# Kernel tuning notes

Measured on AMD Instinct MI355X. Metric: run time of the kernel, lower is better.

## Reference

```python
import jax, jax.numpy as jnp
import numpy as np

B, S, H, HD = 8, 1024, 16, 64
D = H * HD
NINF = -10000.0
EPS = 1e-6


def setup_inputs() -> dict:
    key = jax.random.key(0)
    ks = jax.random.split(key, 6)
    std = 0.02
    return {
        "x": jax.random.normal(ks[0], (B, S, D), jnp.float32),
        "mask": jax.random.randint(ks[1], (B, S), 0, 2, jnp.int32),
        "wq": jax.random.normal(ks[2], (D, D), jnp.float32) * std,
        "bq": jnp.zeros((D,), jnp.float32),
        "wk": jax.random.normal(ks[3], (D, D), jnp.float32) * std,
        "bk": jnp.zeros((D,), jnp.float32),
        "wv": jax.random.normal(ks[4], (D, D), jnp.float32) * std,
        "bv": jnp.zeros((D,), jnp.float32),
        "wo": jax.random.normal(ks[5], (D, D), jnp.float32) * std,
        "bo": jnp.zeros((D,), jnp.float32),
        "gamma": jnp.ones((D,), jnp.float32),
        "beta": jnp.zeros((D,), jnp.float32),
    }


def _heads(t):
    # [B,S,D] -> [B,H,S,HD]
    return t.reshape(t.shape[0], t.shape[1], H, HD).transpose(0, 2, 1, 3)


def _layernorm(x, gamma, beta):
    mu = jnp.mean(x, -1, keepdims=True)
    var = jnp.mean(jnp.square(x - mu), -1, keepdims=True)
    return (x - mu) * jax.lax.rsqrt(var + EPS) * gamma + beta


def reference(x, mask, wq, bq, wk, bk, wv, bv, wo, bo, gamma, beta):
    q = _heads(x @ wq + bq)
    k = _heads(x @ wk + bk)
    v = _heads(x @ wv + bv)
    scores = jnp.einsum("bhqd,bhkd->bhqk", q, k) / np.sqrt(HD).astype(np.float32)
    # padding mask broadcast over key axis: 1 = masked
    scores = scores + mask.astype(jnp.float32)[:, None, None, :] * NINF
    attn = jax.nn.softmax(scores, axis=-1)
    ctx = jnp.einsum("bhqk,bhkd->bhqd", attn, v)  # [B,H,S,HD]
    ctx = ctx.transpose(0, 2, 1, 3).reshape(B, S, D)
    out = _layernorm(x + ctx @ wo + bo, gamma, beta)
    return out
```

## Files before the change

### kernel.cpp

```cpp
#include <hip/hip_runtime.h>
#include <stdint.h>

typedef unsigned short u16;
typedef unsigned int u32;
typedef __bf16 b16x8 __attribute__((ext_vector_type(8)));
typedef float f32x4 __attribute__((ext_vector_type(4)));

#define B_ 8
#define S_ 1024
#define H_ 16
#define HD_ 64
#define D_ 1024
#define M_ 8192

__device__ __forceinline__ u16 f2bf(float f) {
  u32 u = __float_as_uint(f);
  return (u16)((u + 0x7fffu + ((u >> 16) & 1u)) >> 16);
}
__device__ __forceinline__ u16 bfbits(float f) {
  union {
    __bf16 b;
    u16 u;
  } c;
  c.b = (__bf16)f;
  return c.u;
}

__device__ __forceinline__ f32x4 mfma16(b16x8 a, b16x8 b, f32x4 c) {
  return __builtin_amdgcn_mfma_f32_16x16x32_bf16(a, b, c, 0, 0, 0);
}

__device__ __forceinline__ void cp16(const u16* g, u16* l) {
  __builtin_amdgcn_global_load_lds(
      (const __attribute__((address_space(1))) u32*)(g),
      (__attribute__((address_space(3))) u32*)(l), 16, 0, 0);
}

__global__ __launch_bounds__(1024) void wconv_kernel(
    const float* __restrict__ w0, const float* __restrict__ w1,
    const float* __restrict__ w2, const float* __restrict__ w3,
    u16* __restrict__ t0, u16* __restrict__ t1, u16* __restrict__ t2,
    u16* __restrict__ t3) {
  __shared__ float tile[32][33];
  const int z = blockIdx.z;
  const float* src = (z == 0) ? w0 : (z == 1) ? w1 : (z == 2) ? w2 : w3;
  u16* dst = (z == 0) ? t0 : (z == 1) ? t1 : (z == 2) ? t2 : t3;
  const int tx = threadIdx.x, ty = threadIdx.y;
  const int x0 = blockIdx.x * 32, y0 = blockIdx.y * 32;
  tile[ty][tx] = src[(size_t)(y0 + ty) * D_ + x0 + tx];
  __syncthreads();
  dst[(size_t)(x0 + ty) * D_ + y0 + tx] = f2bf(tile[tx][ty]);
}

__global__ __launch_bounds__(256) void xconv_kernel(const float* __restrict__ x,
                                                    u16* __restrict__ xb) {
  const size_t i = ((size_t)blockIdx.x * 256 + threadIdx.x) * 4;
  const float4 v = *(const float4*)(x + i);
  u16 o[4] = {f2bf(v.x), f2bf(v.y), f2bf(v.z), f2bf(v.w)};
  uint2 pack;
  pack.x = ((u32)o[1] << 16) | o[0];
  pack.y = ((u32)o[3] << 16) | o[2];
  *(uint2*)(xb + i) = pack;
}

#define BM_ 256
#define BN_ 128
#define BK_ 64
#define ABUF_ 16384
#define BBUF_ 8192
#define BUFSZ_ (ABUF_ + BBUF_)

__device__ __forceinline__ void gemm256x128_mainloop(
    const u16* __restrict__ A, const u16* __restrict__ BT, int K, int m0,
    int n0, u16* lds, f32x4 (&acc)[8][2]) {
  const int t = threadIdx.x;
  const int lane = t & 63;
  const int l15 = lane & 15;
  const int q4 = lane >> 4;
  const int w = t >> 6;
  const int wm = w >> 2;
  const int wn = w & 3;

  const f32x4 zero = {0.f, 0.f, 0.f, 0.f};
#pragma unroll
  for (int mt = 0; mt < 8; ++mt)
#pragma unroll
    for (int nt = 0; nt < 2; ++nt) acc[mt][nt] = zero;

  const int rbase = t >> 3;
  const int scol = ((t & 7) ^ (rbase & 7)) * 8;
  const u16* Ag = A + (size_t)(m0 + rbase) * K + scol;
  const u16* Bg = BT + (size_t)(n0 + rbase) * K + scol;
  const int sx = l15 & 7;

  auto STAGE = [&](int kt, int bufi) {
    u16* Ab = lds + bufi * BUFSZ_;
    u16* Bb = Ab + ABUF_;
    const int k0 = kt * BK_;
#pragma unroll
    for (int c = 0; c < 4; ++c)
      cp16(Ag + (size_t)(c * 64) * K + k0, Ab + c * 4096 + t * 8);
#pragma unroll
    for (int c = 0; c < 2; ++c)
      cp16(Bg + (size_t)(c * 64) * K + k0, Bb + c * 4096 + t * 8);
  };

  const int NT = K / BK_;
  STAGE(0, 0);
  STAGE(1, 1);

  int cur = 0;
  for (int kt = 0; kt < NT; ++kt) {
    if (kt + 2 < NT) {
      int nb = cur + 2;
      if (nb >= 3) nb -= 3;
      STAGE(kt + 2, nb);
    }
    if (kt + 2 < NT)
      asm volatile("s_waitcnt vmcnt(12)" ::: "memory");
    else if (kt + 1 < NT)
      asm volatile("s_waitcnt vmcnt(6)" ::: "memory");
    else
      asm volatile("s_waitcnt vmcnt(0)" ::: "memory");
    asm volatile("s_barrier" ::: "memory");

    const u16* Ab = lds + cur * BUFSZ_;
    const u16* Bb = Ab + ABUF_;

#pragma unroll
    for (int kk = 0; kk < 2; ++kk) {
      b16x8 af[8], bf2[2];
      const int cc = ((kk * 4 + q4) ^ sx) * 8;
#pragma unroll
      for (int mt = 0; mt < 8; ++mt)
        af[mt] = *(const b16x8*)(Ab + (wm * 128 + mt * 16 + l15) * 64 + cc);
#pragma unroll
      for (int nt = 0; nt < 2; ++nt)
        bf2[nt] = *(const b16x8*)(Bb + (wn * 32 + nt * 16 + l15) * 64 + cc);
      asm volatile("s_barrier" ::: "memory");
      __builtin_amdgcn_s_setprio(1);
#pragma unroll
      for (int mt = 0; mt < 8; ++mt) {
        acc[mt][0] = mfma16(af[mt], bf2[0], acc[mt][0]);
        acc[mt][1] = mfma16(af[mt], bf2[1], acc[mt][1]);
      }
      __builtin_amdgcn_s_setprio(0);
      asm volatile("s_barrier" ::: "memory");
    }
    ++cur;
    if (cur == 3) cur = 0;
  }
}

__global__ __launch_bounds__(512, 2) void qkv_gemm_kernel(
    const u16* __restrict__ xb, const u16* __restrict__ wt3,
    const float* __restrict__ bq, const float* __restrict__ bk,
    const float* __restrict__ bv, u16* __restrict__ Q, u16* __restrict__ Kb,
    u16* __restrict__ VT) {
  __shared__ __align__(16) u16 lds[3 * BUFSZ_];
  const int wg = blockIdx.x;
  const int xcd = wg & 7;
  const int s = wg >> 3;
  const int by = xcd * 4 + (s & 3);
  const int bx = s >> 2;
  const int m0 = by * 256;
  const int n0 = bx * 128;

  f32x4 acc[8][2];
  gemm256x128_mainloop(xb, wt3, D_, m0, n0, lds, acc);

  const int t = threadIdx.x;
  const int lane = t & 63, w = t >> 6;
  const int l15 = lane & 15, q4 = lane >> 4;
  const int wm = w >> 2, wn = w & 3;

  const int z = n0 >> 10;
  u16* out = (z == 0) ? Q : (z == 1) ? Kb : VT;
  const float* bias = (z == 0) ? bq : (z == 1) ? bk : bv;

  for (int nt = 0; nt < 2; ++nt) {
    const int nf = n0 + wn * 32 + nt * 16 + l15;
    const int n1 = nf & 1023;
    const float bias_v = bias[n1];
    const int h = n1 >> 6, hd = n1 & 63;
    for (int mt = 0; mt < 8; ++mt) {
      for (int r = 0; r < 4; ++r) {
        const int m = m0 + wm * 128 + mt * 16 + q4 * 4 + r;
        const int b = m >> 10, ss = m & 1023;
        const float v = acc[mt][nt][r] + bias_v;
        size_t idx;
        if (z < 2)
          idx = (((size_t)(b * H_ + h)) * S_ + ss) * HD_ + hd;
        else
          idx = (((size_t)(b * H_ + h)) * HD_ + hd) * S_ + ss;
        out[idx] = f2bf(v);
      }
    }
  }
}

#define PAD_ 68
#define QPAD_ 72
__global__ __launch_bounds__(256) void attn_kernel(
    const u16* __restrict__ Q, const u16* __restrict__ Kb,
    const u16* __restrict__ VT, const int* __restrict__ mask,
    u16* __restrict__ ctx) {
  __shared__ __align__(16) u16 QPlds[64 * QPAD_];
  __shared__ __align__(16) u16 Klds[64 * PAD_];
  __shared__ __align__(16) u16 Vlds[64 * PAD_];
  __shared__ __align__(16) float Mlds[1024];

  const int t = threadIdx.x;
  const int lane = t & 63, w = t >> 6;
  const int l15 = lane & 15, q4 = lane >> 4;
  const int id = blockIdx.x;
  const int bh = id & 127;
  const int b = bh >> 4, h = bh & 15;
  const int q0 = (id >> 7) * 64;

  const u16* Qbh = Q + (size_t)bh * S_ * HD_;
  const u16* Kbh = Kb + (size_t)bh * S_ * HD_;
  const u16* Vbh = VT + (size_t)bh * S_ * HD_;
  const int* maskb = mask + b * S_;

  const int srow = t >> 3, scol = (t & 7) * 8;
  {
    b16x8 q0v = *(const b16x8*)(Qbh + (size_t)(q0 + srow) * HD_ + scol);
    b16x8 q1v = *(const b16x8*)(Qbh + (size_t)(q0 + srow + 32) * HD_ + scol);
    const int4 mv = *(const int4*)(maskb + t * 4);
    *(b16x8*)(QPlds + srow * QPAD_ + scol) = q0v;
    *(b16x8*)(QPlds + (srow + 32) * QPAD_ + scol) = q1v;
    float4 mf;
    mf.x = -14427.0f * (float)mv.x;
    mf.y = -14427.0f * (float)mv.y;
    mf.z = -14427.0f * (float)mv.z;
    mf.w = -14427.0f * (float)mv.w;
    *(float4*)(Mlds + t * 4) = mf;
  }
  __syncthreads();
  b16x8 aq[2];
  aq[0] = *(const b16x8*)(QPlds + (w * 16 + l15) * QPAD_ + q4 * 8);
  aq[1] = *(const b16x8*)(QPlds + (w * 16 + l15) * QPAD_ + 32 + q4 * 8);

  const f32x4 zero = {0.f, 0.f, 0.f, 0.f};
  f32x4 acc[4];
  for (int nt = 0; nt < 4; ++nt) acc[nt] = zero;
  float lsum = 0.f;
  u16* Pw = QPlds + w * 16 * QPAD_;
  const float c1 = 0.18033688f;

  b16x8 kv0 = *(const b16x8*)(Kbh + (size_t)srow * HD_ + scol);
  b16x8 kv1 = *(const b16x8*)(Kbh + (size_t)(srow + 32) * HD_ + scol);
  b16x8 vv0 = *(const b16x8*)(Vbh + (size_t)srow * S_ + scol);
  b16x8 vv1 = *(const b16x8*)(Vbh + (size_t)(srow + 32) * S_ + scol);

  for (int j = 0; j < 16; ++j) {
    const int key0 = j * 64;
    __syncthreads();
    *(b16x8*)(Klds + srow * PAD_ + scol) = kv0;
    *(b16x8*)(Klds + (srow + 32) * PAD_ + scol) = kv1;
    *(b16x8*)(Vlds + srow * PAD_ + scol) = vv0;
    *(b16x8*)(Vlds + (srow + 32) * PAD_ + scol) = vv1;
    __syncthreads();

    if (j < 15) {
      const int kn = key0 + 64;
      kv0 = *(const b16x8*)(Kbh + (size_t)(kn + srow) * HD_ + scol);
      kv1 = *(const b16x8*)(Kbh + (size_t)(kn + srow + 32) * HD_ + scol);
      vv0 = *(const b16x8*)(Vbh + (size_t)srow * S_ + kn + scol);
      vv1 = *(const b16x8*)(Vbh + (size_t)(srow + 32) * S_ + kn + scol);
    }

    f32x4 sf[4];
    for (int nt = 0; nt < 4; ++nt) sf[nt] = zero;
    for (int kk = 0; kk < 2; ++kk)
      for (int nt = 0; nt < 4; ++nt) {
        b16x8 bk =
            *(const b16x8*)(Klds + (nt * 16 + l15) * PAD_ + kk * 32 + q4 * 8);
        sf[nt] = mfma16(bk, aq[kk], sf[nt]);
      }

    for (int nt = 0; nt < 4; ++nt) {
      const float4 mk = *(const float4*)(Mlds + key0 + nt * 16 + q4 * 4);
      float p0 = __builtin_amdgcn_exp2f(sf[nt][0] * c1 + mk.x);
      float p1 = __builtin_amdgcn_exp2f(sf[nt][1] * c1 + mk.y);
      float p2 = __builtin_amdgcn_exp2f(sf[nt][2] * c1 + mk.z);
      float p3 = __builtin_amdgcn_exp2f(sf[nt][3] * c1 + mk.w);
      lsum += (p0 + p1) + (p2 + p3);
      uint2 pk;
      pk.x = ((u32)bfbits(p1) << 16) | bfbits(p0);
      pk.y = ((u32)bfbits(p3) << 16) | bfbits(p2);
      *(uint2*)(Pw + l15 * QPAD_ + nt * 16 + q4 * 4) = pk;
    }
    asm volatile("s_waitcnt lgkmcnt(0)" ::: "memory");

    for (int kk = 0; kk < 2; ++kk) {
      b16x8 bp = *(const b16x8*)(Pw + l15 * QPAD_ + kk * 32 + q4 * 8);
      for (int nt = 0; nt < 4; ++nt) {
        b16x8 vb =
            *(const b16x8*)(Vlds + (nt * 16 + l15) * PAD_ + kk * 32 + q4 * 8);
        acc[nt] = mfma16(vb, bp, acc[nt]);
      }
    }
  }

  lsum += __shfl_xor(lsum, 16);
  lsum += __shfl_xor(lsum, 32);
  const float inv = 1.0f / lsum;

  const int srw = q0 + w * 16 + l15;
  u16* crow = ctx + ((size_t)(b * S_ + srw)) * D_ + h * 64;
  for (int nt = 0; nt < 4; ++nt) {
    uint2 pk;
    pk.x = ((u32)bfbits(acc[nt][1] * inv) << 16) | bfbits(acc[nt][0] * inv);
    pk.y = ((u32)bfbits(acc[nt][3] * inv) << 16) | bfbits(acc[nt][2] * inv);
    *(uint2*)(crow + nt * 16 + q4 * 4) = pk;
  }
}

__global__ __launch_bounds__(512, 2) void out_gemm_kernel(
    const u16* __restrict__ ctx, const u16* __restrict__ wto,
    const float* __restrict__ bo, const float* __restrict__ x,
    float* __restrict__ y) {
  __shared__ __align__(16) u16 lds[3 * BUFSZ_];
  const int wg = blockIdx.x;
  const int xcd = wg & 7;
  const int s = wg >> 3;
  const int by = xcd * 4 + (s & 3);
  const int bx = s >> 2;
  const int m0 = by * 256, n0 = bx * 128;

  f32x4 acc[8][2];
  gemm256x128_mainloop(ctx, wto, D_, m0, n0, lds, acc);

  const int t = threadIdx.x;
  const int lane = t & 63, w = t >> 6;
  const int l15 = lane & 15, q4 = lane >> 4;
  const int wm = w >> 2, wn = w & 3;

  for (int nt = 0; nt < 2; ++nt) {
    const int n = n0 + wn * 32 + nt * 16 + l15;
    const float bias = bo[n];
    for (int mt = 0; mt < 8; ++mt) {
      for (int r = 0; r < 4; ++r) {
        const int m = m0 + wm * 128 + mt * 16 + q4 * 4 + r;
        y[(size_t)m * D_ + n] = acc[mt][nt][r] + bias + x[(size_t)m * D_ + n];
      }
    }
  }
}

__global__ __launch_bounds__(256) void ln_kernel(const float* __restrict__ y,
                                                 const float* __restrict__ g,
                                                 const float* __restrict__ be,
                                                 float* __restrict__ out) {
  const int row = blockIdx.x, t = threadIdx.x;
  const float* yr = y + (size_t)row * D_;
  const float4 v = *(const float4*)(yr + t * 4);
  float s = v.x + v.y + v.z + v.w;
  float ss = v.x * v.x + v.y * v.y + v.z * v.z + v.w * v.w;
  for (int off = 1; off < 64; off <<= 1) {
    s += __shfl_xor(s, off);
    ss += __shfl_xor(ss, off);
  }
  __shared__ float red[8];
  const int w = t >> 6, lane = t & 63;
  if (lane == 0) {
    red[w] = s;
    red[4 + w] = ss;
  }
  __syncthreads();
  s = red[0] + red[1] + red[2] + red[3];
  ss = red[4] + red[5] + red[6] + red[7];
  const float mu = s * (1.f / 1024.f);
  const float var = ss * (1.f / 1024.f) - mu * mu;
  const float rs = rsqrtf(var + 1e-6f);
  const int c = t * 4;
  const float4 gv = *(const float4*)(g + c);
  const float4 bv = *(const float4*)(be + c);
  float4 o;
  o.x = (v.x - mu) * rs * gv.x + bv.x;
  o.y = (v.y - mu) * rs * gv.y + bv.y;
  o.z = (v.z - mu) * rs * gv.z + bv.z;
  o.w = (v.w - mu) * rs * gv.w + bv.w;
  *(float4*)(out + (size_t)row * D_ + c) = o;
}

extern "C" void kernel_launch(void* const* d_in, const int* in_sizes, int n_in,
                              void* d_out, int out_size, void* d_ws,
                              size_t ws_size, hipStream_t stream) {
  const float* x = (const float*)d_in[0];
  const int* mask = (const int*)d_in[1];
  const float* wq = (const float*)d_in[2];
  const float* bq = (const float*)d_in[3];
  const float* wk = (const float*)d_in[4];
  const float* bk = (const float*)d_in[5];
  const float* wv = (const float*)d_in[6];
  const float* bv = (const float*)d_in[7];
  const float* wo = (const float*)d_in[8];
  const float* bo = (const float*)d_in[9];
  const float* gamma = (const float*)d_in[10];
  const float* beta = (const float*)d_in[11];
  float* out = (float*)d_out;

  char* ws = (char*)d_ws;
  const size_t MB = 1024ull * 1024ull;
  u16* wtq = (u16*)(ws + 0 * MB);
  u16* wtk = (u16*)(ws + 2 * MB);
  u16* wtv = (u16*)(ws + 4 * MB);
  u16* wto = (u16*)(ws + 6 * MB);
  u16* xb = (u16*)(ws + 8 * MB);
  u16* ctx = (u16*)(ws + 8 * MB);
  u16* Qb = (u16*)(ws + 24 * MB);
  u16* Kb = (u16*)(ws + 40 * MB);
  u16* VTb = (u16*)(ws + 56 * MB);
  float* y = (float*)(ws + 24 * MB);

  wconv_kernel<<<dim3(32, 32, 4), dim3(32, 32), 0, stream>>>(
      wq, wk, wv, wo, wtq, wtk, wtv, wto);
  xconv_kernel<<<8192, 256, 0, stream>>>(x, xb);
  qkv_gemm_kernel<<<768, 512, 0, stream>>>(xb, wtq, bq, bk, bv, Qb, Kb, VTb);
  attn_kernel<<<2048, 256, 0, stream>>>(Qb, Kb, VTb, mask, ctx);
  out_gemm_kernel<<<256, 512, 0, stream>>>(ctx, wto, bo, x, y);
  ln_kernel<<<8192, 256, 0, stream>>>(y, gamma, beta, out);
}
```

Before: 301.6 us.

## Use 256x256 tiles with interleaved quadrant prefetch in QKV GEMM

```diff
diff --git a/kernel.cpp b/kernel.cpp
--- a/kernel.cpp
+++ b/kernel.cpp
@@ -63,29 +63,22 @@
   *(uint2*)(xb + i) = pack;
 }
 
-#define BM_ 256
-#define BN_ 128
-#define BK_ 64
-#define ABUF_ 16384
-#define BBUF_ 8192
-#define BUFSZ_ (ABUF_ + BBUF_)
-
-__device__ __forceinline__ void gemm256x128_mainloop(
-    const u16* __restrict__ A, const u16* __restrict__ BT, int K, int m0,
-    int n0, u16* lds, f32x4 (&acc)[8][2]) {
+__device__ __forceinline__ void gemm256sq_mainloop(
+    const u16* __restrict__ A, const u16* __restrict__ BT, int m0, int n0,
+    u16* lds, f32x4 (&acc)[8][4]) {
   const int t = threadIdx.x;
   const int lane = t & 63;
-  const int l15 = lane & 15;
-  const int q4 = lane >> 4;
+  const int l15 = lane & 15, q4 = lane >> 4;
   const int w = t >> 6;
   const int wm = w >> 2;
   const int wn = w & 3;
+  const int K = D_;
 
   const f32x4 zero = {0.f, 0.f, 0.f, 0.f};
 #pragma unroll
-  for (int mt = 0; mt < 8; ++mt)
-#pragma unroll
-    for (int nt = 0; nt < 2; ++nt) acc[mt][nt] = zero;
+  for (int mf = 0; mf < 8; ++mf)
+#pragma unroll
+    for (int nf = 0; nf < 4; ++nf) acc[mf][nf] = zero;
 
   const int rbase = t >> 3;
   const int scol = ((t & 7) ^ (rbase & 7)) * 8;
@@ -93,62 +86,124 @@
   const u16* Bg = BT + (size_t)(n0 + rbase) * K + scol;
   const int sx = l15 & 7;
 
-  auto STAGE = [&](int kt, int bufi) {
-    u16* Ab = lds + bufi * BUFSZ_;
-    u16* Bb = Ab + ABUF_;
-    const int k0 = kt * BK_;
-#pragma unroll
-    for (int c = 0; c < 4; ++c)
-      cp16(Ag + (size_t)(c * 64) * K + k0, Ab + c * 4096 + t * 8);
-#pragma unroll
-    for (int c = 0; c < 2; ++c)
-      cp16(Bg + (size_t)(c * 64) * K + k0, Bb + c * 4096 + t * 8);
-  };
-
-  const int NT = K / BK_;
-  STAGE(0, 0);
-  STAGE(1, 1);
-
-  int cur = 0;
-  for (int kt = 0; kt < NT; ++kt) {
-    if (kt + 2 < NT) {
-      int nb = cur + 2;
-      if (nb >= 3) nb -= 3;
-      STAGE(kt + 2, nb);
-    }
-    if (kt + 2 < NT)
-      asm volatile("s_waitcnt vmcnt(12)" ::: "memory");
-    else if (kt + 1 < NT)
-      asm volatile("s_waitcnt vmcnt(6)" ::: "memory");
+  const int alo = wm * 2 * 4096 + l15 * 64;
+  const int ahi = (wm * 2 + 1) * 4096 + l15 * 64;
+  const int bbase = 16384 + wn * 4096 + l15 * 64;
+  const int cc0 = ((0 + q4) ^ sx) * 8;
+  const int cc1 = ((4 + q4) ^ sx) * 8;
+
+  cp16(Bg, lds + 16384 + t * 8);
+  cp16(Bg + 64 * K, lds + 16384 + 4096 + t * 8);
+  cp16(Bg + 128 * K, lds + 16384 + 8192 + t * 8);
+  cp16(Bg + 192 * K, lds + 16384 + 12288 + t * 8);
+  cp16(Ag, lds + t * 8);
+  cp16(Ag + 128 * K, lds + 8192 + t * 8);
+  cp16(Ag + 64 * K, lds + 4096 + t * 8);
+  cp16(Ag + 192 * K, lds + 12288 + t * 8);
+
+#pragma unroll 1
+  for (int kt = 0; kt < 16; ++kt) {
+    u16* cb = lds + (kt & 1) * 32768;
+    u16* nb = lds + ((kt + 1) & 1) * 32768;
+    const int k1 = (kt + 1) * 64;
+    const bool pf = (kt < 15);
+
+    b16x8 af[4][2], bf[2][2];
+
+    asm volatile("s_waitcnt vmcnt(2)" ::: "memory");
+    asm volatile("s_barrier" ::: "memory");
+#pragma unroll
+    for (int mf = 0; mf < 4; ++mf) {
+      af[mf][0] = *(const b16x8*)(cb + alo + mf * 1024 + cc0);
+      af[mf][1] = *(const b16x8*)(cb + alo + mf * 1024 + cc1);
+    }
+#pragma unroll
+    for (int nf = 0; nf < 2; ++nf) {
+      bf[nf][0] = *(const b16x8*)(cb + bbase + nf * 1024 + cc0);
+      bf[nf][1] = *(const b16x8*)(cb + bbase + nf * 1024 + cc1);
+    }
+    if (pf) {
+      cp16(Bg + k1, nb + 16384 + t * 8);
+      cp16(Bg + 64 * K + k1, nb + 16384 + 4096 + t * 8);
+    }
+    __builtin_amdgcn_s_setprio(1);
+#pragma unroll
+    for (int mf = 0; mf < 4; ++mf)
+#pragma unroll
+      for (int nf = 0; nf < 2; ++nf) {
+        acc[mf][nf] = mfma16(af[mf][0], bf[nf][0], acc[mf][nf]);
+        acc[mf][nf] = mfma16(af[mf][1], bf[nf][1], acc[mf][nf]);
+      }
+    __builtin_amdgcn_s_setprio(0);
+
+    asm volatile("s_barrier" ::: "memory");
+#pragma unroll
+    for (int nf = 0; nf < 2; ++nf) {
+      bf[nf][0] = *(const b16x8*)(cb + bbase + (nf + 2) * 1024 + cc0);
+      bf[nf][1] = *(const b16x8*)(cb + bbase + (nf + 2) * 1024 + cc1);
+    }
+    if (pf) {
+      cp16(Bg + 128 * K + k1, nb + 16384 + 8192 + t * 8);
+      cp16(Bg + 192 * K + k1, nb + 16384 + 12288 + t * 8);
+    }
+    __builtin_amdgcn_s_setprio(1);
+#pragma unroll
+    for (int mf = 0; mf < 4; ++mf)
+#pragma unroll
+      for (int nf = 0; nf < 2; ++nf) {
+        acc[mf][nf + 2] = mfma16(af[mf][0], bf[nf][0], acc[mf][nf + 2]);
+        acc[mf][nf + 2] = mfma16(af[mf][1], bf[nf][1], acc[mf][nf + 2]);
+      }
+    __builtin_amdgcn_s_setprio(0);
+
+    if (pf)
+      asm volatile("s_waitcnt vmcnt(4)" ::: "memory");
     else
       asm volatile("s_waitcnt vmcnt(0)" ::: "memory");
     asm volatile("s_barrier" ::: "memory");
-
-    const u16* Ab = lds + cur * BUFSZ_;
-    const u16* Bb = Ab + ABUF_;
-
-#pragma unroll
-    for (int kk = 0; kk < 2; ++kk) {
-      b16x8 af[8], bf2[2];
-      const int cc = ((kk * 4 + q4) ^ sx) * 8;
-#pragma unroll
-      for (int mt = 0; mt < 8; ++mt)
-        af[mt] = *(const b16x8*)(Ab + (wm * 128 + mt * 16 + l15) * 64 + cc);
-#pragma unroll
-      for (int nt = 0; nt < 2; ++nt)
-        bf2[nt] = *(const b16x8*)(Bb + (wn * 32 + nt * 16 + l15) * 64 + cc);
-      asm volatile("s_barrier" ::: "memory");
-      __builtin_amdgcn_s_setprio(1);
-#pragma unroll
-      for (int mt = 0; mt < 8; ++mt) {
-        acc[mt][0] = mfma16(af[mt], bf2[0], acc[mt][0]);
-        acc[mt][1] = mfma16(af[mt], bf2[1], acc[mt][1]);
-      }
-      __builtin_amdgcn_s_setprio(0);
-      asm volatile("s_barrier" ::: "memory");
-    }
-    ++cur;
-    if (cur == 3) cur = 0;
+#pragma unroll
+    for (int mf = 0; mf < 4; ++mf) {
+      af[mf][0] = *(const b16x8*)(cb + ahi + mf * 1024 + cc0);
+      af[mf][1] = *(const b16x8*)(cb + ahi + mf * 1024 + cc1);
+    }
+#pragma unroll
+    for (int nf = 0; nf < 2; ++nf) {
+      bf[nf][0] = *(const b16x8*)(cb + bbase + nf * 1024 + cc0);
+      bf[nf][1] = *(const b16x8*)(cb + bbase + nf * 1024 + cc1);
+    }
+    if (pf) {
+      cp16(Ag + k1, nb + t * 8);
+      cp16(Ag + 128 * K + k1, nb + 8192 + t * 8);
+    }
+    __builtin_amdgcn_s_setprio(1);
+#pragma unroll
+    for (int mf = 0; mf < 4; ++mf)
+#pragma unroll
+      for (int nf = 0; nf < 2; ++nf) {
+        acc[mf + 4][nf] = mfma16(af[mf][0], bf[nf][0], acc[mf + 4][nf]);
+        acc[mf + 4][nf] = mfma16(af[mf][1], bf[nf][1], acc[mf + 4][nf]);
+      }
+    __builtin_amdgcn_s_setprio(0);
+
+    asm volatile("s_barrier" ::: "memory");
+#pragma unroll
+    for (int nf = 0; nf < 2; ++nf) {
+      bf[nf][0] = *(const b16x8*)(cb + bbase + (nf + 2) * 1024 + cc0);
+      bf[nf][1] = *(const b16x8*)(cb + bbase + (nf + 2) * 1024 + cc1);
+    }
+    if (pf) {
+      cp16(Ag + 64 * K + k1, nb + 4096 + t * 8);
+      cp16(Ag + 192 * K + k1, nb + 12288 + t * 8);
+    }
+    __builtin_amdgcn_s_setprio(1);
+#pragma unroll
+    for (int mf = 0; mf < 4; ++mf)
+#pragma unroll
+      for (int nf = 0; nf < 2; ++nf) {
+        acc[mf + 4][nf + 2] = mfma16(af[mf][0], bf[nf][0], acc[mf + 4][nf + 2]);
+        acc[mf + 4][nf + 2] = mfma16(af[mf][1], bf[nf][1], acc[mf + 4][nf + 2]);
+      }
+    __builtin_amdgcn_s_setprio(0);
   }
 }
 
@@ -157,17 +212,17 @@
     const float* __restrict__ bq, const float* __restrict__ bk,
     const float* __restrict__ bv, u16* __restrict__ Q, u16* __restrict__ Kb,
     u16* __restrict__ VT) {
-  __shared__ __align__(16) u16 lds[3 * BUFSZ_];
+  __shared__ __align__(16) u16 lds[65536];
   const int wg = blockIdx.x;
   const int xcd = wg & 7;
   const int s = wg >> 3;
   const int by = xcd * 4 + (s & 3);
   const int bx = s >> 2;
   const int m0 = by * 256;
-  const int n0 = bx * 128;
-
-  f32x4 acc[8][2];
-  gemm256x128_mainloop(xb, wt3, D_, m0, n0, lds, acc);
+  const int n0 = bx * 256;
+
+  f32x4 acc[8][4];
+  gemm256sq_mainloop(xb, wt3, m0, n0, lds, acc);
 
   const int t = threadIdx.x;
   const int lane = t & 63, w = t >> 6;
@@ -178,8 +233,8 @@
   u16* out = (z == 0) ? Q : (z == 1) ? Kb : VT;
   const float* bias = (z == 0) ? bq : (z == 1) ? bk : bv;
 
-  for (int nt = 0; nt < 2; ++nt) {
-    const int nf = n0 + wn * 32 + nt * 16 + l15;
+  for (int nt = 0; nt < 4; ++nt) {
+    const int nf = n0 + wn * 64 + nt * 16 + l15;
     const int n1 = nf & 1023;
     const float bias_v = bias[n1];
     const int h = n1 >> 6, hd = n1 & 63;
@@ -196,6 +251,92 @@
         out[idx] = f2bf(v);
       }
     }
+  }
+}
+
+#define ABUF_ 16384
+#define BBUF_ 8192
+#define BUFSZ_ (ABUF_ + BBUF_)
+
+__device__ __forceinline__ void gemm256x128_mainloop(
+    const u16* __restrict__ A, const u16* __restrict__ BT, int K, int m0,
+    int n0, u16* lds, f32x4 (&acc)[8][2]) {
+  const int t = threadIdx.x;
+  const int lane = t & 63;
+  const int l15 = lane & 15;
+  const int q4 = lane >> 4;
+  const int w = t >> 6;
+  const int wm = w >> 2;
+  const int wn = w & 3;
+
+  const f32x4 zero = {0.f, 0.f, 0.f, 0.f};
+#pragma unroll
+  for (int mt = 0; mt < 8; ++mt)
+#pragma unroll
+    for (int nt = 0; nt < 2; ++nt) acc[mt][nt] = zero;
+
+  const int rbase = t >> 3;
+  const int scol = ((t & 7) ^ (rbase & 7)) * 8;
+  const u16* Ag = A + (size_t)(m0 + rbase) * K + scol;
+  const u16* Bg = BT + (size_t)(n0 + rbase) * K + scol;
+  const int sx = l15 & 7;
+
+  auto STAGE = [&](int kt, int bufi) {
+    u16* Ab = lds + bufi * BUFSZ_;
+    u16* Bb = Ab + ABUF_;
+    const int k0 = kt * 64;
+#pragma unroll
+    for (int c = 0; c < 4; ++c)
+      cp16(Ag + (size_t)(c * 64) * K + k0, Ab + c * 4096 + t * 8);
+#pragma unroll
+    for (int c = 0; c < 2; ++c)
+      cp16(Bg + (size_t)(c * 64) * K + k0, Bb + c * 4096 + t * 8);
+  };
+
+  const int NT = K / 64;
+  STAGE(0, 0);
+  STAGE(1, 1);
+
+  int cur = 0;
+  for (int kt = 0; kt < NT; ++kt) {
+    if (kt + 2 < NT) {
+      int nb = cur + 2;
+      if (nb >= 3) nb -= 3;
+      STAGE(kt + 2, nb);
+    }
+    if (kt + 2 < NT)
+      asm volatile("s_waitcnt vmcnt(12)" ::: "memory");
+    else if (kt + 1 < NT)
+      asm volatile("s_waitcnt vmcnt(6)" ::: "memory");
+    else
+      asm volatile("s_waitcnt vmcnt(0)" ::: "memory");
+    asm volatile("s_barrier" ::: "memory");
+
+    const u16* Ab = lds + cur * BUFSZ_;
+    const u16* Bb = Ab + ABUF_;
+
+#pragma unroll
+    for (int kk = 0; kk < 2; ++kk) {
+      b16x8 af[8], bf2[2];
+      const int cc = ((kk * 4 + q4) ^ sx) * 8;
+#pragma unroll
+      for (int mt = 0; mt < 8; ++mt)
+        af[mt] = *(const b16x8*)(Ab + (wm * 128 + mt * 16 + l15) * 64 + cc);
+#pragma unroll
+      for (int nt = 0; nt < 2; ++nt)
+        bf2[nt] = *(const b16x8*)(Bb + (wn * 32 + nt * 16 + l15) * 64 + cc);
+      asm volatile("s_barrier" ::: "memory");
+      __builtin_amdgcn_s_setprio(1);
+#pragma unroll
+      for (int mt = 0; mt < 8; ++mt) {
+        acc[mt][0] = mfma16(af[mt], bf2[0], acc[mt][0]);
+        acc[mt][1] = mfma16(af[mt], bf2[1], acc[mt][1]);
+      }
+      __builtin_amdgcn_s_setprio(0);
+      asm volatile("s_barrier" ::: "memory");
+    }
+    ++cur;
+    if (cur == 3) cur = 0;
   }
 }
 
@@ -419,7 +560,7 @@
   wconv_kernel<<<dim3(32, 32, 4), dim3(32, 32), 0, stream>>>(
       wq, wk, wv, wo, wtq, wtk, wtv, wto);
   xconv_kernel<<<8192, 256, 0, stream>>>(x, xb);
-  qkv_gemm_kernel<<<768, 512, 0, stream>>>(xb, wtq, bq, bk, bv, Qb, Kb, VTb);
+  qkv_gemm_kernel<<<384, 512, 0, stream>>>(xb, wtq, bq, bk, bv, Qb, Kb, VTb);
   attn_kernel<<<2048, 256, 0, stream>>>(Qb, Kb, VTb, mask, ctx);
   out_gemm_kernel<<<256, 512, 0, stream>>>(ctx, wto, bo, x, y);
   ln_kernel<<<8192, 256, 0, stream>>>(y, gamma, beta, out);
```

Result: slower. 372.3 us (+23.4%).
